# Performance work log

Measured on AMD Instinct MI355X. Metric: run time of the kernel, lower is better.

## Reference

```python
import jax, jax.numpy as jnp
import numpy as np

TWO_PI = 2.0 * np.pi


def dht3(x):
    """Faithful port of the 3D branch of dht(): x is (D, M, N).
    NOTE: the original does x.view(D, N, M) -- a RESHAPE, not a transpose --
    which we reproduce exactly with jnp.reshape (both are row-major).
    """
    D, M, N = x.shape
    n = jnp.arange(N, dtype=x.dtype)
    arg = TWO_PI * n[:, None] * n[None, :] / N
    cas = jnp.cos(arg) + jnp.sin(arg)                      # (N, N)
    xv = x.reshape(D, N, M).transpose(1, 0, 2).reshape(N, D * M)
    X = cas @ xv                                           # (N, D*M)
    return X.reshape(N, D, M).transpose(1, 2, 0)           # (D, M, N)


def compl_mul1d(x1, x2):
    # x1: (B, Cin, modes), x2: (Cin, Cout, modes)
    neg = lambda t: jnp.roll(jnp.flip(t, axis=-1), 1, axis=-1)
    x1n, x2n = neg(x1), neg(x2)
    return 0.5 * (jnp.einsum('bix,iox->box', x1, x2)
                  - jnp.einsum('bix,iox->box', x1n, x2n)
                  + jnp.einsum('bix,iox->box', x1, x2n)
                  + jnp.einsum('bix,iox->box', x1n, x2))


def setup_inputs() -> dict:
    key = jax.random.key(0)
    k1, k2 = jax.random.split(key)
    B, C_in, C_out, N, modes1 = 32, 64, 64, 4096, 64
    x = jax.random.normal(k1, (B, C_in, N), dtype=jnp.float32)
    scale = 1.0 / (C_in * C_out)
    weights1 = scale * jax.random.uniform(k2, (C_in, C_out, modes1), dtype=jnp.float32)
    return {"x": x, "weights1": weights1}


def reference(x, weights1):
    B, C, N = x.shape
    modes1 = weights1.shape[-1]
    x_ht = dht3(x)                           # DHT(x)
    x_ht_flip = dht3(jnp.flip(x, axis=-1))   # DHT(flip(x))
    # phase = angle(complex(cos_part, sin_part)) = atan2(sin, cos)
    phase = jnp.arctan2(x_ht_flip, x_ht)     # (B, C, N)
    K = N // 2 + 1
    out_ht = jnp.zeros((B, C, K), dtype=x.dtype)
    out_ht = out_ht.at[:, :, :modes1].set(compl_mul1d(x_ht[:, :, :modes1], weights1))
    xi = dht3(out_ht) / K                    # idht over length-K last dim
    # original multiplies by cos(phase) of mismatched length; slice to K
    return xi * jnp.cos(phase[:, :, :K])     # (B, C, K)
```

## Files before the change

### kernel.cpp

```cpp
#include <hip/hip_runtime.h>
#include <hip/hip_bf16.h>

typedef __attribute__((ext_vector_type(8))) short short8;
typedef __attribute__((ext_vector_type(4))) float f32x4;

constexpr int NSEQ  = 4096;
constexpr int MROWS = 2049;
constexpr int MPAD  = 2176;
constexpr int KHT   = 2049;
constexpr int TABST = 2080;
constexpr int BATCH = 32;
constexpr int SLABS = 512;
constexpr float TPI = 6.283185307179586f;

constexpr size_t PLANE_USH = (size_t)SLABS * MPAD * 8;

constexpr size_t ASPL_FLT = 3 * PLANE_USH / 2;
constexpr size_t COSP_OFF = ASPL_FLT;
constexpr size_t COSP_SZ  = (size_t)MPAD * 2048;
constexpr size_t XH_OFF   = COSP_OFF + COSP_SZ;
constexpr size_t XH_SZ    = (size_t)64 * 2048;
constexpr size_t TAB_OFF  = XH_OFF + XH_SZ;
constexpr size_t TAB_SZ   = (size_t)128 * TABST;
constexpr size_t OH_OFF   = TAB_OFF + TAB_SZ;

__device__ __forceinline__ void split3(float v, short &h0, short &h1, short &h2) {
  __hip_bfloat16 b0 = __float2bfloat16(v);
  float f0 = __bfloat162float(b0);
  float r1 = v - f0;
  __hip_bfloat16 b1 = __float2bfloat16(r1);
  float f1 = __bfloat162float(b1);
  float r2 = r1 - f1;
  __hip_bfloat16 b2 = __float2bfloat16(r2);
  h0 = __builtin_bit_cast(short, b0);
  h1 = __builtin_bit_cast(short, b1);
  h2 = __builtin_bit_cast(short, b2);
}

__device__ __forceinline__ void gl_lds16(const short* g, short* s) {
  __builtin_amdgcn_global_load_lds((const __attribute__((address_space(1))) void*)g,
                                   (__attribute__((address_space(3))) void*)s, 16, 0, 0);
}

__global__ __launch_bounds__(256) void prep_A(short* __restrict__ Aq) {
  int row = blockIdx.x * 256 + threadIdx.x;
  if (row >= MPAD) return;
  int slab = blockIdx.y;
  short8 o0, o1, o2;
  float t1 = TPI * (float)row;
  #pragma unroll
  for (int e = 0; e < 8; ++e) {
    float v = 0.0f;
    if (row < MROWS) {
      float t2  = t1 * (float)(slab * 8 + e);
      float arg = t2 * (1.0f / 4096.0f);
      v = cosf(arg) + sinf(arg);
    }
    short h0, h1, h2; split3(v, h0, h1, h2);
    o0[e] = h0; o1[e] = h1; o2[e] = h2;
  }
  size_t base = (size_t)slab * (MPAD * 8) + (size_t)row * 8;
  *(short8*)(Aq + base)                  = o0;
  *(short8*)(Aq + PLANE_USH + base)      = o1;
  *(short8*)(Aq + 2 * PLANE_USH + base)  = o2;
}

__global__ __launch_bounds__(256) void prep_tab(float* __restrict__ tab) {
  int idx = blockIdx.x * 256 + threadIdx.x;
  if (idx >= 128 * TABST) return;
  int j  = idx / TABST;
  int np = idx - j * TABST;
  float v = 0.0f;
  if (np < KHT) {
    int c = j >> 1, b = j & 1;
    int pp = 32 * c + b;
    float t1  = TPI * (float)np;
    float t2  = t1 * (float)pp;
    float arg = t2 / 2049.0f;
    v = (cosf(arg) + sinf(arg)) * (1.0f / 2049.0f);
  }
  tab[idx] = v;
}

__global__ __launch_bounds__(256, 2) void gemm_mfma(const short* __restrict__ Aq,
                                                    const float* __restrict__ x,
                                                    float* __restrict__ cosp,
                                                    float* __restrict__ xh64) {
  __shared__ __align__(16) short As[3][4096];
  __shared__ __align__(16) short Bs[3][4096];
  const int t    = threadIdx.x;
  const int lane = t & 63;
  const int w    = t >> 6;
  const int wr   = w >> 1, wc = w & 1;
  const int bm   = blockIdx.y * 128;
  const int c0   = blockIdx.x * 64;

  const int j    = t & 127;
  const int sA   = t >> 7;
  const int cc   = c0 + (j >> 1);
  const int flip = j & 1;
  const int mm   = cc & 63;
  const float* xb = x + (cc >> 6) * 262144;
  const int bi0  = (sA * 128 + j) * 8;
  const int bi1  = ((sA + 2) * 128 + j) * 8;

  int aIdx[4], bIdx[4];
  #pragma unroll
  for (int f = 0; f < 4; ++f) {
    aIdx[f] = (lane >> 4) * 1024 + (wr * 64 + f * 16 + (lane & 15)) * 8;
    bIdx[f] = (lane >> 4) * 1024 + (wc * 64 + f * 16 + (lane & 15)) * 8;
  }

  f32x4 accM[4][4] = {};
  f32x4 accL[4][4] = {};

  for (int k0 = 0; k0 < NSEQ; k0 += 32) {
    const int sg0 = k0 >> 3;
    #pragma unroll
    for (int i = 0; i < 6; ++i) {
      int q = w * 6 + i;
      int p = q >> 3, s = (q >> 1) & 3, h = q & 1;
      const short* gp = Aq + (size_t)p * PLANE_USH + (size_t)(sg0 + s) * (MPAD * 8)
                        + (size_t)(bm + h * 64 + lane) * 8;
      gl_lds16(gp, &As[p][s * 1024 + h * 512]);
    }
    #pragma unroll
    for (int tk = 0; tk < 2; ++tk) {
      int s  = (tk == 0) ? sA : sA + 2;
      int kb = k0 + s * 8;
      int hi = (kb >> 6) << 12;
      int lo = ((kb & 63) << 6) + mm;
      int base = flip ? (hi + 4095 - lo) : (hi + lo);
      int step = flip ? -64 : 64;
      short8 p0, p1, p2;
      #pragma unroll
      for (int e = 0; e < 8; ++e) {
        float v = xb[base + e * step];
        short h0, h1, h2; split3(v, h0, h1, h2);
        p0[e] = h0; p1[e] = h1; p2[e] = h2;
      }
      int bi = (tk == 0) ? bi0 : bi1;
      *(short8*)&Bs[0][bi] = p0;
      *(short8*)&Bs[1][bi] = p1;
      *(short8*)&Bs[2][bi] = p2;
    }
    __syncthreads();

    short8 fa0[4], fa1[4], fa2[4];
    #pragma unroll
    for (int f = 0; f < 4; ++f) {
      fa0[f] = *(const short8*)&As[0][aIdx[f]];
      fa1[f] = *(const short8*)&As[1][aIdx[f]];
      fa2[f] = *(const short8*)&As[2][aIdx[f]];
    }
    {
      short8 fb[4];
      #pragma unroll
      for (int f = 0; f < 4; ++f) fb[f] = *(const short8*)&Bs[0][bIdx[f]];
      #pragma unroll
      for (int fi = 0; fi < 4; ++fi)
        #pragma unroll
        for (int fj = 0; fj < 4; ++fj) {
          accM[fi][fj] = __builtin_amdgcn_mfma_f32_16x16x32_bf16(fa0[fi], fb[fj], accM[fi][fj], 0, 0, 0);
          accL[fi][fj] = __builtin_amdgcn_mfma_f32_16x16x32_bf16(fa1[fi], fb[fj], accL[fi][fj], 0, 0, 0);
          accL[fi][fj] = __builtin_amdgcn_mfma_f32_16x16x32_bf16(fa2[fi], fb[fj], accL[fi][fj], 0, 0, 0);
        }
    }
    {
      short8 fb[4];
      #pragma unroll
      for (int f = 0; f < 4; ++f) fb[f] = *(const short8*)&Bs[1][bIdx[f]];
      #pragma unroll
      for (int fi = 0; fi < 4; ++fi)
        #pragma unroll
        for (int fj = 0; fj < 4; ++fj) {
          accL[fi][fj] = __builtin_amdgcn_mfma_f32_16x16x32_bf16(fa0[fi], fb[fj], accL[fi][fj], 0, 0, 0);
          accL[fi][fj] = __builtin_amdgcn_mfma_f32_16x16x32_bf16(fa1[fi], fb[fj], accL[fi][fj], 0, 0, 0);
        }
    }
    {
      short8 fb[4];
      #pragma unroll
      for (int f = 0; f < 4; ++f) fb[f] = *(const short8*)&Bs[2][bIdx[f]];
      #pragma unroll
      for (int fi = 0; fi < 4; ++fi)
        #pragma unroll
        for (int fj = 0; fj < 4; ++fj)
          accL[fi][fj] = __builtin_amdgcn_mfma_f32_16x16x32_bf16(fa0[fi], fb[fj], accL[fi][fj], 0, 0, 0);
    }
    __syncthreads();
  }

  #pragma unroll
  for (int fi = 0; fi < 4; ++fi) {
    int row0 = bm + wr * 64 + fi * 16 + ((lane >> 4) << 2);
    #pragma unroll
    for (int fj = 0; fj < 4; ++fj) {
      int jc = wc * 64 + fj * 16 + (lane & 15);
      int c  = c0 + (jc >> 1);
      #pragma unroll
      for (int r = 0; r < 4; ++r) {
        float v = accM[fi][fj][r] + accL[fi][fj][r];
        float o = __shfl_xor(v, 1, 64);
        float a = (lane & 1) ? o : v;
        float b = (lane & 1) ? v : o;
        float r2 = a * a + b * b;
        float cp = (r2 > 0.0f) ? (a / sqrtf(r2)) : 1.0f;
        if ((lane & 1) == 0) {
          cosp[(size_t)(row0 + r) * 2048 + c] = cp;
          if (bm == 0 && wr == 0) xh64[(row0 + r) * 2048 + c] = a;
        }
      }
    }
  }
}

__global__ __launch_bounds__(256) void complmul(const float* __restrict__ xh64,
                                                const float* __restrict__ W,
                                                float* __restrict__ oh) {
  __shared__ float cl[64 * 65];
  const int t  = threadIdx.x;
  const int bq = blockIdx.y;
  const int og = blockIdx.x;
  #pragma unroll
  for (int e = 0; e < 16; ++e) {
    int idx = t + e * 256;
    int i = idx & 63, m = idx >> 6;
    cl[m * 65 + i] = xh64[m * 2048 + bq * 64 + i];
  }
  __syncthreads();
  const int m  = t & 63;
  const int o  = og * 4 + (t >> 6);
  const int mn = (64 - m) & 63;
  float s = 0.0f;
  for (int i = 0; i < 64; ++i) {
    float w  = W[i * 4096 + o * 64 + m];
    float wn = W[i * 4096 + o * 64 + mn];
    s += cl[m * 65 + i] * (w + wn) + cl[mn * 65 + i] * (w - wn);
  }
  oh[bq * 4096 + o * 64 + m] = 0.5f * s;
}

__global__ __launch_bounds__(256) void final_k(const float* __restrict__ cosp,
                                               const float* __restrict__ tab,
                                               const float* __restrict__ oh,
                                               float* __restrict__ out) {
  __shared__ float tl[128 * 32];
  __shared__ float ol[64 * 64];
  const int t  = threadIdx.x;
  const int d  = blockIdx.y;
  const int n0 = blockIdx.x * 32;
  #pragma unroll
  for (int e = 0; e < 16; ++e) {
    int idx = t + e * 256;
    tl[idx] = tab[(idx >> 5) * TABST + n0 + (idx & 31)];
  }
  #pragma unroll
  for (int e = 0; e < 16; ++e) {
    int idx = t + e * 256;
    ol[idx] = oh[d * 4096 + idx];
  }
  __syncthreads();
  const int mp   = t & 63;
  const int nsub = t >> 6;

  float ohreg[64];
  #pragma unroll
  for (int c = 0; c < 64; ++c)
    ohreg[c] = ol[c * 64 + ((mp - c) & 63)];

  float acc[8] = {};
  #pragma unroll
  for (int c = 0; c < 64; ++c) {
    const float* tp = &tl[(2 * c + (c > mp ? 1 : 0)) * 32 + nsub * 8];
    float tv[8];
    *(float4*)&tv[0] = *(const float4*)tp;
    *(float4*)&tv[4] = *(const float4*)(tp + 4);
    #pragma unroll
    for (int q = 0; q < 8; ++q) acc[q] += tv[q] * ohreg[c];
  }
  #pragma unroll
  for (int q = 0; q < 8; ++q) {
    int np = n0 + nsub * 8 + q;
    if (np < KHT) {
      float cp = cosp[(size_t)np * 2048 + d * 64 + mp];
      out[d * 131136 + mp * 2049 + np] = acc[q] * cp;
    }
  }
}

extern "C" void kernel_launch(void* const* d_in, const int* in_sizes, int n_in,
                              void* d_out, int out_size, void* d_ws, size_t ws_size,
                              hipStream_t stream) {
  const float* x = (const float*)d_in[0];
  const float* W = (const float*)d_in[1];
  float* out = (float*)d_out;
  float* ws  = (float*)d_ws;

  short* Aq    = (short*)ws;
  float* cospB = ws + COSP_OFF;
  float* xh64  = ws + XH_OFF;
  float* tab   = ws + TAB_OFF;
  float* oh    = ws + OH_OFF;

  prep_A   <<<dim3((MPAD + 255) / 256, SLABS), dim3(256), 0, stream>>>(Aq);
  prep_tab <<<dim3((128 * TABST + 255) / 256), dim3(256), 0, stream>>>(tab);
  gemm_mfma<<<dim3(32, 17), dim3(256), 0, stream>>>(Aq, x, cospB, xh64);
  complmul <<<dim3(16, BATCH), dim3(256), 0, stream>>>(xh64, W, oh);
  final_k  <<<dim3(65, BATCH), dim3(256), 0, stream>>>(cospB, tab, oh, out);
}
```

Baseline: 878.6 us.

## Double-buffer A tiles and prefetch B into registers in MFMA GEMM loop

The main DHT GEMM loop now double-buffers the A tile in LDS and prefetches the next B tile's x values into registers while the current tile's MFMAs run, so global load latency overlaps with compute. It also raises wave priority around the MFMA block. The bf16 three-way split now uses truncation via bit masks instead of round-to-nearest conversions, which is cheaper but gives a slightly different residual split. The cost is twice the LDS for A, which may lower occupancy, plus extra registers for the prefetched values.

```diff
diff --git a/kernel.cpp b/kernel.cpp
--- a/kernel.cpp
+++ b/kernel.cpp
@@ -24,17 +24,17 @@
 constexpr size_t TAB_SZ   = (size_t)128 * TABST;
 constexpr size_t OH_OFF   = TAB_OFF + TAB_SZ;
 
-__device__ __forceinline__ void split3(float v, short &h0, short &h1, short &h2) {
-  __hip_bfloat16 b0 = __float2bfloat16(v);
-  float f0 = __bfloat162float(b0);
+__device__ __forceinline__ void split3t(float v, short &h0, short &h1, short &h2) {
+  unsigned u  = __builtin_bit_cast(unsigned, v);
+  unsigned u0 = u & 0xFFFF0000u;
+  float f0 = __builtin_bit_cast(float, u0);
   float r1 = v - f0;
-  __hip_bfloat16 b1 = __float2bfloat16(r1);
-  float f1 = __bfloat162float(b1);
+  unsigned u1 = __builtin_bit_cast(unsigned, r1) & 0xFFFF0000u;
+  float f1 = __builtin_bit_cast(float, u1);
   float r2 = r1 - f1;
-  __hip_bfloat16 b2 = __float2bfloat16(r2);
-  h0 = __builtin_bit_cast(short, b0);
-  h1 = __builtin_bit_cast(short, b1);
-  h2 = __builtin_bit_cast(short, b2);
+  h0 = (short)(u0 >> 16);
+  h1 = (short)(u1 >> 16);
+  h2 = (short)(__builtin_bit_cast(unsigned, r2) >> 16);
 }
 
 __device__ __forceinline__ void gl_lds16(const short* g, short* s) {
@@ -56,7 +56,7 @@
       float arg = t2 * (1.0f / 4096.0f);
       v = cosf(arg) + sinf(arg);
     }
-    short h0, h1, h2; split3(v, h0, h1, h2);
+    short h0, h1, h2; split3t(v, h0, h1, h2);
     o0[e] = h0; o1[e] = h1; o2[e] = h2;
   }
   size_t base = (size_t)slab * (MPAD * 8) + (size_t)row * 8;
@@ -86,7 +86,7 @@
                                                     const float* __restrict__ x,
                                                     float* __restrict__ cosp,
                                                     float* __restrict__ xh64) {
-  __shared__ __align__(16) short As[3][4096];
+  __shared__ __align__(16) short As[2][3][4096];
   __shared__ __align__(16) short Bs[3][4096];
   const int t    = threadIdx.x;
   const int lane = t & 63;
@@ -113,30 +113,39 @@
 
   f32x4 accM[4][4] = {};
   f32x4 accL[4][4] = {};
-
-  for (int k0 = 0; k0 < NSEQ; k0 += 32) {
-    const int sg0 = k0 >> 3;
+  float breg[16];
+
+  auto issueA = [&](int kt, int buf) {
+    const int sg0 = kt << 2;
     #pragma unroll
     for (int i = 0; i < 6; ++i) {
       int q = w * 6 + i;
       int p = q >> 3, s = (q >> 1) & 3, h = q & 1;
       const short* gp = Aq + (size_t)p * PLANE_USH + (size_t)(sg0 + s) * (MPAD * 8)
                         + (size_t)(bm + h * 64 + lane) * 8;
-      gl_lds16(gp, &As[p][s * 1024 + h * 512]);
-    }
+      gl_lds16(gp, &As[buf][p][s * 1024 + h * 512]);
+    }
+  };
+  auto issueB = [&](int kt) {
     #pragma unroll
     for (int tk = 0; tk < 2; ++tk) {
       int s  = (tk == 0) ? sA : sA + 2;
-      int kb = k0 + s * 8;
+      int kb = kt * 32 + s * 8;
       int hi = (kb >> 6) << 12;
       int lo = ((kb & 63) << 6) + mm;
       int base = flip ? (hi + 4095 - lo) : (hi + lo);
       int step = flip ? -64 : 64;
+      #pragma unroll
+      for (int e = 0; e < 8; ++e) breg[tk * 8 + e] = xb[base + e * step];
+    }
+  };
+  auto writeB = [&]() {
+    #pragma unroll
+    for (int tk = 0; tk < 2; ++tk) {
       short8 p0, p1, p2;
       #pragma unroll
       for (int e = 0; e < 8; ++e) {
-        float v = xb[base + e * step];
-        short h0, h1, h2; split3(v, h0, h1, h2);
+        short h0, h1, h2; split3t(breg[tk * 8 + e], h0, h1, h2);
         p0[e] = h0; p1[e] = h1; p2[e] = h2;
       }
       int bi = (tk == 0) ? bi0 : bi1;
@@ -144,15 +153,16 @@
       *(short8*)&Bs[1][bi] = p1;
       *(short8*)&Bs[2][bi] = p2;
     }
-    __syncthreads();
-
+  };
+  auto compute = [&](int buf) {
     short8 fa0[4], fa1[4], fa2[4];
     #pragma unroll
     for (int f = 0; f < 4; ++f) {
-      fa0[f] = *(const short8*)&As[0][aIdx[f]];
-      fa1[f] = *(const short8*)&As[1][aIdx[f]];
-      fa2[f] = *(const short8*)&As[2][aIdx[f]];
-    }
+      fa0[f] = *(const short8*)&As[buf][0][aIdx[f]];
+      fa1[f] = *(const short8*)&As[buf][1][aIdx[f]];
+      fa2[f] = *(const short8*)&As[buf][2][aIdx[f]];
+    }
+    __builtin_amdgcn_s_setprio(1);
     {
       short8 fb[4];
       #pragma unroll
@@ -188,6 +198,20 @@
         for (int fj = 0; fj < 4; ++fj)
           accL[fi][fj] = __builtin_amdgcn_mfma_f32_16x16x32_bf16(fa0[fi], fb[fj], accL[fi][fj], 0, 0, 0);
     }
+    __builtin_amdgcn_s_setprio(0);
+  };
+
+  issueA(0, 0);
+  issueB(0);
+  writeB();
+  __syncthreads();
+
+  for (int kt = 0; kt < 128; ++kt) {
+    int nb = kt + 1;
+    if (nb < 128) { issueA(nb, nb & 1); issueB(nb); }
+    compute(kt & 1);
+    __syncthreads();
+    if (nb < 128) writeB();
     __syncthreads();
   }
 
```

Measured after the change: 937.6 us. 6.7% more time.
